# Kernel optimization log

Measured on AMD Instinct MI355X. Metric: run time of the kernel, lower is better.

## Reference

```python
import jax, jax.numpy as jnp
from jax import lax
import numpy as np

DN = ('NCHW', 'OIHW', 'NCHW')

def conv_reflect(x, w, b, pad):
    # torch Conv2d with padding_mode='reflect': reflect-pad then valid conv
    x = jnp.pad(x, ((0, 0), (0, 0), (pad, pad), (pad, pad)), mode='reflect')
    y = lax.conv_general_dilated(x, w, (1, 1), 'VALID', dimension_numbers=DN)
    return y + b[None, :, None, None]

def setup_inputs() -> dict:
    key = jax.random.key(0)
    ks = jax.random.split(key, 8)
    B, W, H = 4, 1024, 1024
    inp = {
        'input': jax.random.normal(ks[0], (B, 12, W, H), dtype=jnp.float32),
        'w1': jax.random.normal(ks[1], (32, 12, 7, 7), dtype=jnp.float32) * 0.05,
        'b1': jnp.zeros((32,), dtype=jnp.float32),
        'w2': jax.random.normal(ks[2], (32, 32, 5, 5), dtype=jnp.float32) * 0.05,
        'b2': jnp.zeros((32,), dtype=jnp.float32),
        'w3': jax.random.normal(ks[3], (8, 32, 5, 5), dtype=jnp.float32) * 0.05,
        'b3': jnp.zeros((8,), dtype=jnp.float32),
        'dwkernel': jax.random.normal(ks[4], (8, 1, 7, 7), dtype=jnp.float32),
    }
    return inp

def reference(input, w1, b1, w2, b2, w3, b3, dwkernel):
    B, _, W, H = input.shape
    color = input[:, 0:3]
    albedo = input[:, 3:6]
    albedo = jnp.where(albedo < 0.001, jnp.float32(1.0), albedo)
    color = color / albedo
    net_in = jnp.concatenate([color, albedo, input[:, 6:]], axis=1)  # (B,12,W,H)

    h = jax.nn.relu(conv_reflect(net_in, w1, b1, 3))
    h = jax.nn.relu(conv_reflect(h, w2, b2, 2))
    logits = conv_reflect(h, w3, b3, 2)  # (B,8,W,H)
    kernel = jax.nn.softmax(logits / 5.0, axis=1)  # (B,8,W,H)

    # grouped conv: dwkernel repeated over 3 color channels, zero padding=3
    rpk = jnp.tile(dwkernel, (3, 1, 1, 1))  # (24,1,7,7)
    preconv = lax.conv_general_dilated(
        color, rpk, (1, 1), [(3, 3), (3, 3)],
        dimension_numbers=DN, feature_group_count=3,
    )  # (B,24,W,H)
    preconv = preconv.reshape(B, 3, 8, W, H)

    # (kernel expanded over color dim * preconv).sum over kernel dim
    filtered = jnp.einsum('bkwh,bckwh->bcwh', kernel, preconv)
    remodulated = albedo * filtered
    return remodulated
```

## Files before the change

kernel.cpp:

```cpp
#include <hip/hip_runtime.h>

#define IMG 1024

typedef _Float16 half8 __attribute__((ext_vector_type(8)));
typedef float f32x4 __attribute__((ext_vector_type(4)));

__device__ __forceinline__ int refl(int i) {
    i = (i < 0) ? -i : i;
    return (i >= IMG) ? (2 * IMG - 2 - i) : i;
}
__device__ __forceinline__ float afix(float a) { return (a < 0.001f) ? 1.0f : a; }
__device__ __forceinline__ int iclamp(int v, int lo, int hi) { return v < lo ? lo : (v > hi ? hi : v); }
__device__ __forceinline__ int swz64(int a) { return a ^ (((((a >> 6) & 3) ^ ((a >> 8) & 1)) << 4)); }
__device__ __forceinline__ int swz32(int a) { return a ^ ((((a >> 7) & 1)) << 4); }
__device__ __forceinline__ unsigned short h2b(_Float16 h) { union { _Float16 f; unsigned short u; } x; x.f = h; return x.u; }

__global__ void wprep_kernel(const float* __restrict__ w1, const float* __restrict__ w2,
                             const float* __restrict__ w3,
                             char* __restrict__ w1p, char* __restrict__ w2p, char* __restrict__ w3p)
{
    const int NF1 = 7 * 2 * 4 * 2, NF2 = 5 * 2 * 5 * 2, NF3 = 5 * 5 * 2;
    int gid = blockIdx.x * 256 + threadIdx.x;
    int f = gid >> 6, l = gid & 63;
    if (f >= NF1 + NF2 + NF3) return;
    int r = l & 15, g = l >> 4;
    half8 out;
    char* dst;
    if (f < NF1) {
        int pl = f & 1, j = (f >> 1) & 3, oct = (f >> 3) & 1, ky = f >> 4;
        int oc = oct * 16 + r;
#pragma unroll
        for (int e = 0; e < 8; e++) {
            int k = g * 8 + e, kx = 2 * j + (k >> 4), ic = k & 15;
            float v = (ic < 12 && kx < 7) ? w1[((oc * 12 + ic) * 7 + ky) * 7 + kx] : 0.f;
            _Float16 h = (_Float16)v;
            out[e] = pl ? (_Float16)(v - (float)h) : h;
        }
        dst = w1p + (size_t)f * 1024 + l * 16;
    } else if (f < NF1 + NF2) {
        int ff = f - NF1;
        int pl = ff & 1, t2 = ff >> 1;
        int kx = t2 % 5; t2 /= 5;
        int oct = t2 & 1, ky = t2 >> 1;
        int oc = oct * 16 + r;
#pragma unroll
        for (int e = 0; e < 8; e++) {
            int ic = g * 8 + e;
            float v = w2[((oc * 32 + ic) * 5 + ky) * 5 + kx];
            _Float16 h = (_Float16)v;
            out[e] = pl ? (_Float16)(v - (float)h) : h;
        }
        dst = w2p + (size_t)ff * 1024 + l * 16;
    } else {
        int ff = f - NF1 - NF2;
        int pl = ff & 1, t2 = ff >> 1;
        int kx = t2 % 5, ky = t2 / 5;
#pragma unroll
        for (int e = 0; e < 8; e++) {
            int ic = g * 8 + e;
            float v = (r < 8) ? w3[((r * 32 + ic) * 5 + ky) * 5 + kx] : 0.f;
            _Float16 h = (_Float16)v;
            out[e] = pl ? (_Float16)(v - (float)h) : h;
        }
        dst = w3p + (size_t)ff * 1024 + l * 16;
    }
    *(half8*)dst = out;
}

__global__ void netin_kernel(const float* __restrict__ in, char* __restrict__ nh, char* __restrict__ nl)
{
    const int M = IMG * IMG;
    int px = blockIdx.x * 256 + threadIdx.x;
    float v[16];
#pragma unroll
    for (int c = 0; c < 3; c++) {
        float a = afix(in[(size_t)(c + 3) * M + px]);
        v[c] = (in[(size_t)c * M + px] / a) * 0.25f;
        v[c + 3] = a * 0.25f;
    }
#pragma unroll
    for (int c = 6; c < 12; c++) v[c] = in[(size_t)c * M + px] * 0.25f;
#pragma unroll
    for (int c = 12; c < 16; c++) v[c] = 0.f;
    unsigned short hb[16], lb[16];
#pragma unroll
    for (int c = 0; c < 16; c++) {
        _Float16 h = (_Float16)v[c];
        hb[c] = h2b(h);
        lb[c] = h2b((_Float16)(v[c] - (float)h));
    }
    *(int4*)(nh + (size_t)px * 32) = *(int4*)&hb[0];
    *(int4*)(nh + (size_t)px * 32 + 16) = *(int4*)&hb[8];
    *(int4*)(nl + (size_t)px * 32) = *(int4*)&lb[0];
    *(int4*)(nl + (size_t)px * 32 + 16) = *(int4*)&lb[8];
}

__global__ __launch_bounds__(256, 2) void conv1_mfma(
    const char* __restrict__ nh, const char* __restrict__ nl,
    const char* __restrict__ w1p, const float* __restrict__ b1,
    char* __restrict__ h1h, char* __restrict__ h1l, int a1, int e1)
{
    __shared__ __align__(16) char sm[2 * 14 * 1280];
    const int t = threadIdx.x, l = t & 63, w = t >> 6;
    const int c = l & 15, g = l >> 4;
    const int x0 = blockIdx.x * 32;
    const int ystart = a1 + blockIdx.y * 8;

    for (int q = t; q < 2240; q += 256) {
        int pl = q / 1120, rem = q % 1120;
        int slab = rem / 80, c2 = rem % 80;
        int px = c2 >> 1, s = c2 & 1;
        int gy = refl(ystart + slab - 3);
        int gx = refl(x0 + px - 3);
        const char* src = (pl ? nl : nh) + ((size_t)gy * IMG + gx) * 32 + s * 16;
        *(int4*)(sm + pl * 17920 + slab * 1280 + swz32(px * 32 + s * 16)) = *(const int4*)src;
    }
    __syncthreads();

    f32x4 zero4 = {0.f, 0.f, 0.f, 0.f};
    f32x4 acc[2][4];
#pragma unroll
    for (int o = 0; o < 2; o++)
#pragma unroll
        for (int r = 0; r < 4; r++) acc[o][r] = zero4;

    const int pxt = w & 1, rbase = (w >> 1) * 4;
#pragma unroll 1
    for (int ky = 0; ky < 7; ky++) {
        half8 aw[2][4][2];
#pragma unroll
        for (int oct = 0; oct < 2; oct++)
#pragma unroll
            for (int j = 0; j < 4; j++)
#pragma unroll
                for (int pl = 0; pl < 2; pl++)
                    aw[oct][j][pl] = *(const half8*)(w1p + (size_t)((((ky * 2 + oct) * 4 + j) * 2 + pl)) * 1024 + l * 16);
#pragma unroll
        for (int r = 0; r < 4; r++) {
            const char* base = sm + (rbase + r + ky) * 1280;
#pragma unroll
            for (int j = 0; j < 4; j++) {
                int p2 = pxt * 16 + c + 2 * j + (g >> 1);
                int off = swz32(p2 * 32 + (g & 1) * 16);
                half8 bh = *(const half8*)(base + off);
                half8 bl = *(const half8*)(base + 17920 + off);
#pragma unroll
                for (int oct = 0; oct < 2; oct++) {
                    acc[oct][r] = __builtin_amdgcn_mfma_f32_16x16x32_f16(aw[oct][j][0], bh, acc[oct][r], 0, 0, 0);
                    acc[oct][r] = __builtin_amdgcn_mfma_f32_16x16x32_f16(aw[oct][j][0], bl, acc[oct][r], 0, 0, 0);
                    acc[oct][r] = __builtin_amdgcn_mfma_f32_16x16x32_f16(aw[oct][j][1], bh, acc[oct][r], 0, 0, 0);
                }
            }
        }
    }
#pragma unroll
    for (int r = 0; r < 4; r++) {
        int y = ystart + rbase + r;
        if (y < e1) {
            int x = x0 + pxt * 16 + c, ybuf = y - a1;
#pragma unroll
            for (int oct = 0; oct < 2; oct++) {
                ushort4 hv, lv;
                float vv[4];
#pragma unroll
                for (int i = 0; i < 4; i++) {
                    int oc = oct * 16 + g * 4 + i;
                    float v = acc[oct][r][i] * 4.f + b1[oc];
                    vv[i] = fmaxf(v, 0.f) * 0.125f;
                }
                _Float16 h0 = (_Float16)vv[0], h1_ = (_Float16)vv[1], h2_ = (_Float16)vv[2], h3 = (_Float16)vv[3];
                hv.x = h2b(h0); hv.y = h2b(h1_); hv.z = h2b(h2_); hv.w = h2b(h3);
                lv.x = h2b((_Float16)(vv[0] - (float)h0)); lv.y = h2b((_Float16)(vv[1] - (float)h1_));
                lv.z = h2b((_Float16)(vv[2] - (float)h2_)); lv.w = h2b((_Float16)(vv[3] - (float)h3));
                size_t ob = ((size_t)ybuf * IMG + x) * 64 + oct * 32 + g * 8;
                *(ushort4*)(h1h + ob) = hv;
                *(ushort4*)(h1l + ob) = lv;
            }
        }
    }
}

__global__ __launch_bounds__(256, 2) void conv2_mfma(
    const char* __restrict__ h1h, const char* __restrict__ h1l,
    const char* __restrict__ w2p, const float* __restrict__ b2,
    char* __restrict__ h2h, char* __restrict__ h2l,
    int a1, int e1, int a2, int e2)
{
    __shared__ __align__(16) char sm[2 * 12 * 2304];
    const int t = threadIdx.x, l = t & 63, w = t >> 6;
    const int c = l & 15, g = l >> 4;
    const int x0 = blockIdx.x * 32;
    const int ystart = a2 + blockIdx.y * 8;

    for (int q = t; q < 3456; q += 256) {
        int pl = q / 1728, rem = q % 1728;
        int slab = rem / 144, c2 = rem % 144;
        int px = c2 >> 2, s = c2 & 3;
        int yy = iclamp(refl(ystart + slab - 2), a1, e1 - 1) - a1;
        int gx = refl(x0 + px - 2);
        const char* src = (pl ? h1l : h1h) + ((size_t)yy * IMG + gx) * 64 + s * 16;
        *(int4*)(sm + pl * 27648 + slab * 2304 + swz64(px * 64 + s * 16)) = *(const int4*)src;
    }
    __syncthreads();

    f32x4 zero4 = {0.f, 0.f, 0.f, 0.f};
    f32x4 acc[2][4];
#pragma unroll
    for (int o = 0; o < 2; o++)
#pragma unroll
        for (int r = 0; r < 4; r++) acc[o][r] = zero4;

    const int pxt = w & 1, rbase = (w >> 1) * 4;
#pragma unroll 1
    for (int ky = 0; ky < 5; ky++) {
        half8 aw[2][5][2];
#pragma unroll
        for (int oct = 0; oct < 2; oct++)
#pragma unroll
            for (int kx = 0; kx < 5; kx++)
#pragma unroll
                for (int pl = 0; pl < 2; pl++)
                    aw[oct][kx][pl] = *(const half8*)(w2p + (size_t)((((ky * 2 + oct) * 5 + kx) * 2 + pl)) * 1024 + l * 16);
#pragma unroll
        for (int r = 0; r < 4; r++) {
            const char* base = sm + (rbase + r + ky) * 2304;
#pragma unroll
            for (int kx = 0; kx < 5; kx++) {
                int p = pxt * 16 + c + kx;
                int off = swz64(p * 64 + g * 16);
                half8 bh = *(const half8*)(base + off);
                half8 bl = *(const half8*)(base + 27648 + off);
#pragma unroll
                for (int oct = 0; oct < 2; oct++) {
                    acc[oct][r] = __builtin_amdgcn_mfma_f32_16x16x32_f16(aw[oct][kx][0], bh, acc[oct][r], 0, 0, 0);
                    acc[oct][r] = __builtin_amdgcn_mfma_f32_16x16x32_f16(aw[oct][kx][0], bl, acc[oct][r], 0, 0, 0);
                    acc[oct][r] = __builtin_amdgcn_mfma_f32_16x16x32_f16(aw[oct][kx][1], bh, acc[oct][r], 0, 0, 0);
                }
            }
        }
    }
#pragma unroll
    for (int r = 0; r < 4; r++) {
        int y = ystart + rbase + r;
        if (y < e2) {
            int x = x0 + pxt * 16 + c, ybuf = y - a2;
#pragma unroll
            for (int oct = 0; oct < 2; oct++) {
                ushort4 hv, lv;
                float vv[4];
#pragma unroll
                for (int i = 0; i < 4; i++) {
                    int oc = oct * 16 + g * 4 + i;
                    float v = acc[oct][r][i] * 8.f + b2[oc];
                    vv[i] = fmaxf(v, 0.f) * 0.125f;
                }
                _Float16 h0 = (_Float16)vv[0], h1_ = (_Float16)vv[1], h2_ = (_Float16)vv[2], h3 = (_Float16)vv[3];
                hv.x = h2b(h0); hv.y = h2b(h1_); hv.z = h2b(h2_); hv.w = h2b(h3);
                lv.x = h2b((_Float16)(vv[0] - (float)h0)); lv.y = h2b((_Float16)(vv[1] - (float)h1_));
                lv.z = h2b((_Float16)(vv[2] - (float)h2_)); lv.w = h2b((_Float16)(vv[3] - (float)h3));
                size_t ob = ((size_t)ybuf * IMG + x) * 64 + oct * 32 + g * 8;
                *(ushort4*)(h2h + ob) = hv;
                *(ushort4*)(h2l + ob) = lv;
            }
        }
    }
}

__global__ __launch_bounds__(256, 2) void conv3_mfma(
    const char* __restrict__ h2h, const char* __restrict__ h2l,
    const char* __restrict__ w3p, const float* __restrict__ b3,
    float* __restrict__ lg, int a2, int e2, int r0, int r1, int rowsL)
{
    __shared__ __align__(16) char sm[2 * 12 * 2304];
    const int t = threadIdx.x, l = t & 63, w = t >> 6;
    const int c = l & 15, g = l >> 4;
    const int x0 = blockIdx.x * 32;
    const int ystart = r0 + blockIdx.y * 8;

    for (int q = t; q < 3456; q += 256) {
        int pl = q / 1728, rem = q % 1728;
        int slab = rem / 144, c2 = rem % 144;
        int px = c2 >> 2, s = c2 & 3;
        int yy = iclamp(refl(ystart + slab - 2), a2, e2 - 1) - a2;
        int gx = refl(x0 + px - 2);
        const char* src = (pl ? h2l : h2h) + ((size_t)yy * IMG + gx) * 64 + s * 16;
        *(int4*)(sm + pl * 27648 + slab * 2304 + swz64(px * 64 + s * 16)) = *(const int4*)src;
    }
    __syncthreads();

    f32x4 zero4 = {0.f, 0.f, 0.f, 0.f};
    f32x4 acc[4];
#pragma unroll
    for (int r = 0; r < 4; r++) acc[r] = zero4;

    const int pxt = w & 1, rbase = (w >> 1) * 4;
#pragma unroll 1
    for (int ky = 0; ky < 5; ky++) {
        half8 aw[5][2];
#pragma unroll
        for (int kx = 0; kx < 5; kx++)
#pragma unroll
            for (int pl = 0; pl < 2; pl++)
                aw[kx][pl] = *(const half8*)(w3p + (size_t)(((ky * 5 + kx) * 2 + pl)) * 1024 + l * 16);
#pragma unroll
        for (int r = 0; r < 4; r++) {
            const char* base = sm + (rbase + r + ky) * 2304;
#pragma unroll
            for (int kx = 0; kx < 5; kx++) {
                int p = pxt * 16 + c + kx;
                int off = swz64(p * 64 + g * 16);
                half8 bh = *(const half8*)(base + off);
                half8 bl = *(const half8*)(base + 27648 + off);
                acc[r] = __builtin_amdgcn_mfma_f32_16x16x32_f16(aw[kx][0], bh, acc[r], 0, 0, 0);
                acc[r] = __builtin_amdgcn_mfma_f32_16x16x32_f16(aw[kx][0], bl, acc[r], 0, 0, 0);
                acc[r] = __builtin_amdgcn_mfma_f32_16x16x32_f16(aw[kx][1], bh, acc[r], 0, 0, 0);
            }
        }
    }
#pragma unroll
    for (int r = 0; r < 4; r++) {
        int y = ystart + rbase + r;
        if (y < r1 && g < 2) {
            int x = x0 + pxt * 16 + c, row = y - r0;
#pragma unroll
            for (int i = 0; i < 4; i++) {
                int oc = g * 4 + i;
                lg[((size_t)oc * rowsL + row) * IMG + x] = acc[r][i] * 8.f + b3[oc];
            }
        }
    }
}

__global__ __launch_bounds__(256, 2) void final_kernel(
    const float* __restrict__ in, const float* __restrict__ lg, const float* __restrict__ dw,
    float* __restrict__ outp, int ylo, int yhi, int rowsL)
{
    __shared__ __align__(16) float sC[3][22][72];
    __shared__ __align__(16) float sdw[8][49];
    const int t = threadIdx.x;
    const int tx = t & 15, ty = t >> 4;
    const int x0 = blockIdx.x * 64;
    const int y0 = ylo + blockIdx.y * 16;

    for (int e = t; e < 8 * 49; e += 256) sdw[e / 49][e % 49] = dw[e];
    for (int e = t; e < 3 * 22 * 70; e += 256) {
        int c = e / (22 * 70), rem = e % (22 * 70);
        int r = rem / 70, cc = rem % 70;
        int gy = y0 + r - 3, gx = x0 + cc - 3;
        float v = 0.f;
        if (gy >= 0 && gy < IMG && gx >= 0 && gx < IMG) {
            float a = afix(in[(size_t)(c + 3) * IMG * IMG + (size_t)gy * IMG + gx]);
            v = in[(size_t)c * IMG * IMG + (size_t)gy * IMG + gx] / a;
        }
        sC[c][r][cc] = v;
    }
    __syncthreads();
    const int y = y0 + ty;
    if (y >= yhi) return;

    float lv[4][8];
#pragma unroll
    for (int k = 0; k < 8; k++) {
        float4 v = *(const float4*)&lg[((size_t)k * rowsL + (y - ylo)) * IMG + x0 + tx * 4];
        lv[0][k] = v.x; lv[1][k] = v.y; lv[2][k] = v.z; lv[3][k] = v.w;
    }
    float p[4][8];
#pragma unroll
    for (int j = 0; j < 4; j++) {
        float m = -3.4e38f;
#pragma unroll
        for (int k = 0; k < 8; k++) m = fmaxf(m, lv[j][k]);
        float s = 0.f;
#pragma unroll
        for (int k = 0; k < 8; k++) { float ev = __expf((lv[j][k] - m) * 0.2f); p[j][k] = ev; s += ev; }
        float invs = 1.0f / s;
#pragma unroll
        for (int k = 0; k < 8; k++) p[j][k] *= invs;
    }

    float filt[3][4];
#pragma unroll
    for (int c = 0; c < 3; c++)
#pragma unroll
        for (int j = 0; j < 4; j++) filt[c][j] = 0.f;

#pragma unroll 1
    for (int ky = 0; ky < 7; ky++) {
        float cv[3][10];
#pragma unroll
        for (int c = 0; c < 3; c++)
#pragma unroll
            for (int jj = 0; jj < 10; jj++) cv[c][jj] = sC[c][ty + ky][tx * 4 + jj];
#pragma unroll
        for (int kx = 0; kx < 7; kx++) {
            float dwv[8];
#pragma unroll
            for (int k = 0; k < 8; k++) dwv[k] = sdw[k][ky * 7 + kx];
#pragma unroll
            for (int j = 0; j < 4; j++) {
                float e0 = 0.f;
#pragma unroll
                for (int k = 0; k < 8; k++) e0 = fmaf(p[j][k], dwv[k], e0);
#pragma unroll
                for (int c = 0; c < 3; c++) filt[c][j] = fmaf(e0, cv[c][kx + j], filt[c][j]);
            }
        }
    }
#pragma unroll
    for (int c = 0; c < 3; c++) {
        const float* ap = &in[(size_t)(c + 3) * IMG * IMG + (size_t)y * IMG + x0 + tx * 4];
        float4 a4 = *(const float4*)ap;
        float4 o4 = make_float4(afix(a4.x) * filt[c][0], afix(a4.y) * filt[c][1],
                                afix(a4.z) * filt[c][2], afix(a4.w) * filt[c][3]);
        *(float4*)&outp[(size_t)c * IMG * IMG + (size_t)y * IMG + x0 + tx * 4] = o4;
    }
}

extern "C" void kernel_launch(void* const* d_in, const int* in_sizes, int n_in,
                              void* d_out, int out_size, void* d_ws, size_t ws_size,
                              hipStream_t stream)
{
    const float* in  = (const float*)d_in[0];
    const float* w1  = (const float*)d_in[1];
    const float* b1  = (const float*)d_in[2];
    const float* w2  = (const float*)d_in[3];
    const float* b2  = (const float*)d_in[4];
    const float* w3  = (const float*)d_in[5];
    const float* b3  = (const float*)d_in[6];
    const float* dw  = (const float*)d_in[7];
    float* out = (float*)d_out;

    const size_t WB1 = 112 * 1024, WB2 = 100 * 1024, WB3 = 50 * 1024;
    const size_t NETIN = (size_t)IMG * IMG * 32;

    int S = 1024;
    while (S > 64) {
        size_t need = WB1 + WB2 + WB3 + 2 * NETIN
                    + 2ull * (S + 8) * IMG * 64 + 2ull * (S + 4) * IMG * 64
                    + (size_t)S * IMG * 8 * 4;
        if (need <= ws_size) break;
        S >>= 1;
    }
    const int rows1 = S + 8, rows2 = S + 4, rowsL = S;

    char* w1p = (char*)d_ws;
    char* w2p = w1p + WB1;
    char* w3p = w2p + WB2;
    char* nh  = w3p + WB3;
    char* nl  = nh + NETIN;
    char* h1h = nl + NETIN;
    char* h1l = h1h + (size_t)rows1 * IMG * 64;
    char* h2h = h1l + (size_t)rows1 * IMG * 64;
    char* h2l = h2h + (size_t)rows2 * IMG * 64;
    float* lgb = (float*)(h2l + (size_t)rows2 * IMG * 64);

    wprep_kernel<<<66, 256, 0, stream>>>(w1, w2, w3, w1p, w2p, w3p);

    for (int b = 0; b < 4; b++) {
        const float* inb = in + (size_t)b * 12 * IMG * IMG;
        float* outb = out + (size_t)b * 3 * IMG * IMG;
        netin_kernel<<<IMG * IMG / 256, 256, 0, stream>>>(inb, nh, nl);
        for (int r0 = 0; r0 < IMG; r0 += S) {
            int r1 = r0 + S; if (r1 > IMG) r1 = IMG;
            int a1 = r0 - 4; if (a1 < 0) a1 = 0;
            int e1 = r1 + 4; if (e1 > IMG) e1 = IMG;
            int a2 = r0 - 2; if (a2 < 0) a2 = 0;
            int e2 = r1 + 2; if (e2 > IMG) e2 = IMG;
            conv1_mfma<<<dim3(32, (e1 - a1 + 7) / 8), 256, 0, stream>>>(nh, nl, w1p, b1, h1h, h1l, a1, e1);
            conv2_mfma<<<dim3(32, (e2 - a2 + 7) / 8), 256, 0, stream>>>(h1h, h1l, w2p, b2, h2h, h2l, a1, e1, a2, e2);
            conv3_mfma<<<dim3(32, (r1 - r0 + 7) / 8), 256, 0, stream>>>(h2h, h2l, w3p, b3, lgb, a2, e2, r0, r1, rowsL);
            final_kernel<<<dim3(16, (r1 - r0 + 15) / 16), 256, 0, stream>>>(inb, lgb, dw, outb, r0, r1, rowsL);
        }
    }
}
```

Baseline: 2.272 ms.

## Split hi/lo activation planes into two sequential LDS passes to halve shared memory

Each conv kernel used to stage both the high and low fp16 planes of its input tile in shared memory at once. Now it stages the high plane, runs the hi×hi and lo-weight×hi MFMAs, then reloads the same buffer with the low plane and runs the hi-weight×lo MFMAs. This halves LDS per block, and launch bounds rise from 2 to 4 blocks per SIMD to buy occupancy. The cost is an extra global-load phase with its own barriers, reloading weights for the second pass, and a tighter register budget that may cause spills.

After: 1.994 ms. 12.2% less time.

```diff
diff --git a/kernel.cpp b/kernel.cpp
--- a/kernel.cpp
+++ b/kernel.cpp
@@ -95,61 +95,87 @@
     *(int4*)(nl + (size_t)px * 32 + 16) = *(int4*)&lb[8];
 }
 
-__global__ __launch_bounds__(256, 2) void conv1_mfma(
+__global__ __launch_bounds__(256, 4) void conv1_mfma(
     const char* __restrict__ nh, const char* __restrict__ nl,
     const char* __restrict__ w1p, const float* __restrict__ b1,
     char* __restrict__ h1h, char* __restrict__ h1l, int a1, int e1)
 {
-    __shared__ __align__(16) char sm[2 * 14 * 1280];
+    __shared__ __align__(16) char sm[14 * 1280];
     const int t = threadIdx.x, l = t & 63, w = t >> 6;
     const int c = l & 15, g = l >> 4;
     const int x0 = blockIdx.x * 32;
     const int ystart = a1 + blockIdx.y * 8;
-
-    for (int q = t; q < 2240; q += 256) {
-        int pl = q / 1120, rem = q % 1120;
-        int slab = rem / 80, c2 = rem % 80;
+    const int pxt = w & 1, rbase = (w >> 1) * 4;
+
+    f32x4 zero4 = {0.f, 0.f, 0.f, 0.f};
+    f32x4 acc[2][4];
+#pragma unroll
+    for (int o = 0; o < 2; o++)
+#pragma unroll
+        for (int r = 0; r < 4; r++) acc[o][r] = zero4;
+
+    for (int q = t; q < 1120; q += 256) {
+        int slab = q / 80, c2 = q % 80;
         int px = c2 >> 1, s = c2 & 1;
         int gy = refl(ystart + slab - 3);
         int gx = refl(x0 + px - 3);
-        const char* src = (pl ? nl : nh) + ((size_t)gy * IMG + gx) * 32 + s * 16;
-        *(int4*)(sm + pl * 17920 + slab * 1280 + swz32(px * 32 + s * 16)) = *(const int4*)src;
-    }
-    __syncthreads();
-
-    f32x4 zero4 = {0.f, 0.f, 0.f, 0.f};
-    f32x4 acc[2][4];
-#pragma unroll
-    for (int o = 0; o < 2; o++)
-#pragma unroll
-        for (int r = 0; r < 4; r++) acc[o][r] = zero4;
-
-    const int pxt = w & 1, rbase = (w >> 1) * 4;
+        *(int4*)(sm + slab * 1280 + swz32(px * 32 + s * 16)) =
+            *(const int4*)(nh + ((size_t)gy * IMG + gx) * 32 + s * 16);
+    }
+    __syncthreads();
 #pragma unroll 1
     for (int ky = 0; ky < 7; ky++) {
-        half8 aw[2][4][2];
+        half8 aw0[2][4], aw1[2][4];
 #pragma unroll
         for (int oct = 0; oct < 2; oct++)
 #pragma unroll
-            for (int j = 0; j < 4; j++)
-#pragma unroll
-                for (int pl = 0; pl < 2; pl++)
-                    aw[oct][j][pl] = *(const half8*)(w1p + (size_t)((((ky * 2 + oct) * 4 + j) * 2 + pl)) * 1024 + l * 16);
+            for (int j = 0; j < 4; j++) {
+                aw0[oct][j] = *(const half8*)(w1p + (size_t)((((ky * 2 + oct) * 4 + j) * 2 + 0)) * 1024 + l * 16);
+                aw1[oct][j] = *(const half8*)(w1p + (size_t)((((ky * 2 + oct) * 4 + j) * 2 + 1)) * 1024 + l * 16);
+            }
 #pragma unroll
         for (int r = 0; r < 4; r++) {
             const char* base = sm + (rbase + r + ky) * 1280;
 #pragma unroll
             for (int j = 0; j < 4; j++) {
                 int p2 = pxt * 16 + c + 2 * j + (g >> 1);
-                int off = swz32(p2 * 32 + (g & 1) * 16);
-                half8 bh = *(const half8*)(base + off);
-                half8 bl = *(const half8*)(base + 17920 + off);
+                half8 bh = *(const half8*)(base + swz32(p2 * 32 + (g & 1) * 16));
 #pragma unroll
                 for (int oct = 0; oct < 2; oct++) {
-                    acc[oct][r] = __builtin_amdgcn_mfma_f32_16x16x32_f16(aw[oct][j][0], bh, acc[oct][r], 0, 0, 0);
-                    acc[oct][r] = __builtin_amdgcn_mfma_f32_16x16x32_f16(aw[oct][j][0], bl, acc[oct][r], 0, 0, 0);
-                    acc[oct][r] = __builtin_amdgcn_mfma_f32_16x16x32_f16(aw[oct][j][1], bh, acc[oct][r], 0, 0, 0);
+                    acc[oct][r] = __builtin_amdgcn_mfma_f32_16x16x32_f16(aw0[oct][j], bh, acc[oct][r], 0, 0, 0);
+                    acc[oct][r] = __builtin_amdgcn_mfma_f32_16x16x32_f16(aw1[oct][j], bh, acc[oct][r], 0, 0, 0);
                 }
+            }
+        }
+    }
+    __syncthreads();
+    for (int q = t; q < 1120; q += 256) {
+        int slab = q / 80, c2 = q % 80;
+        int px = c2 >> 1, s = c2 & 1;
+        int gy = refl(ystart + slab - 3);
+        int gx = refl(x0 + px - 3);
+        *(int4*)(sm + slab * 1280 + swz32(px * 32 + s * 16)) =
+            *(const int4*)(nl + ((size_t)gy * IMG + gx) * 32 + s * 16);
+    }
+    __syncthreads();
+#pragma unroll 1
+    for (int ky = 0; ky < 7; ky++) {
+        half8 aw0[2][4];
+#pragma unroll
+        for (int oct = 0; oct < 2; oct++)
+#pragma unroll
+            for (int j = 0; j < 4; j++)
+                aw0[oct][j] = *(const half8*)(w1p + (size_t)((((ky * 2 + oct) * 4 + j) * 2 + 0)) * 1024 + l * 16);
+#pragma unroll
+        for (int r = 0; r < 4; r++) {
+            const char* base = sm + (rbase + r + ky) * 1280;
+#pragma unroll
+            for (int j = 0; j < 4; j++) {
+                int p2 = pxt * 16 + c + 2 * j + (g >> 1);
+                half8 bl = *(const half8*)(base + swz32(p2 * 32 + (g & 1) * 16));
+#pragma unroll
+                for (int oct = 0; oct < 2; oct++)
+                    acc[oct][r] = __builtin_amdgcn_mfma_f32_16x16x32_f16(aw0[oct][j], bl, acc[oct][r], 0, 0, 0);
             }
         }
     }
@@ -180,62 +206,86 @@
     }
 }
 
-__global__ __launch_bounds__(256, 2) void conv2_mfma(
+__global__ __launch_bounds__(256, 4) void conv2_mfma(
     const char* __restrict__ h1h, const char* __restrict__ h1l,
     const char* __restrict__ w2p, const float* __restrict__ b2,
     char* __restrict__ h2h, char* __restrict__ h2l,
     int a1, int e1, int a2, int e2)
 {
-    __shared__ __align__(16) char sm[2 * 12 * 2304];
+    __shared__ __align__(16) char sm[12 * 2304];
     const int t = threadIdx.x, l = t & 63, w = t >> 6;
     const int c = l & 15, g = l >> 4;
     const int x0 = blockIdx.x * 32;
     const int ystart = a2 + blockIdx.y * 8;
-
-    for (int q = t; q < 3456; q += 256) {
-        int pl = q / 1728, rem = q % 1728;
-        int slab = rem / 144, c2 = rem % 144;
+    const int pxt = w & 1, rbase = (w >> 1) * 4;
+
+    f32x4 zero4 = {0.f, 0.f, 0.f, 0.f};
+    f32x4 acc[2][4];
+#pragma unroll
+    for (int o = 0; o < 2; o++)
+#pragma unroll
+        for (int r = 0; r < 4; r++) acc[o][r] = zero4;
+
+    for (int q = t; q < 1728; q += 256) {
+        int slab = q / 144, c2 = q % 144;
         int px = c2 >> 2, s = c2 & 3;
         int yy = iclamp(refl(ystart + slab - 2), a1, e1 - 1) - a1;
         int gx = refl(x0 + px - 2);
-        const char* src = (pl ? h1l : h1h) + ((size_t)yy * IMG + gx) * 64 + s * 16;
-        *(int4*)(sm + pl * 27648 + slab * 2304 + swz64(px * 64 + s * 16)) = *(const int4*)src;
-    }
-    __syncthreads();
-
-    f32x4 zero4 = {0.f, 0.f, 0.f, 0.f};
-    f32x4 acc[2][4];
-#pragma unroll
-    for (int o = 0; o < 2; o++)
-#pragma unroll
-        for (int r = 0; r < 4; r++) acc[o][r] = zero4;
-
-    const int pxt = w & 1, rbase = (w >> 1) * 4;
+        *(int4*)(sm + slab * 2304 + swz64(px * 64 + s * 16)) =
+            *(const int4*)(h1h + ((size_t)yy * IMG + gx) * 64 + s * 16);
+    }
+    __syncthreads();
 #pragma unroll 1
     for (int ky = 0; ky < 5; ky++) {
-        half8 aw[2][5][2];
+        half8 aw0[2][5], aw1[2][5];
 #pragma unroll
         for (int oct = 0; oct < 2; oct++)
 #pragma unroll
-            for (int kx = 0; kx < 5; kx++)
-#pragma unroll
-                for (int pl = 0; pl < 2; pl++)
-                    aw[oct][kx][pl] = *(const half8*)(w2p + (size_t)((((ky * 2 + oct) * 5 + kx) * 2 + pl)) * 1024 + l * 16);
+            for (int kx = 0; kx < 5; kx++) {
+                aw0[oct][kx] = *(const half8*)(w2p + (size_t)((((ky * 2 + oct) * 5 + kx) * 2 + 0)) * 1024 + l * 16);
+                aw1[oct][kx] = *(const half8*)(w2p + (size_t)((((ky * 2 + oct) * 5 + kx) * 2 + 1)) * 1024 + l * 16);
+            }
 #pragma unroll
         for (int r = 0; r < 4; r++) {
             const char* base = sm + (rbase + r + ky) * 2304;
 #pragma unroll
             for (int kx = 0; kx < 5; kx++) {
-                int p = pxt * 16 + c + kx;
-                int off = swz64(p * 64 + g * 16);
-                half8 bh = *(const half8*)(base + off);
-                half8 bl = *(const half8*)(base + 27648 + off);
+                half8 bh = *(const half8*)(base + swz64((pxt * 16 + c + kx) * 64 + g * 16));
 #pragma unroll
                 for (int oct = 0; oct < 2; oct++) {
-                    acc[oct][r] = __builtin_amdgcn_mfma_f32_16x16x32_f16(aw[oct][kx][0], bh, acc[oct][r], 0, 0, 0);
-                    acc[oct][r] = __builtin_amdgcn_mfma_f32_16x16x32_f16(aw[oct][kx][0], bl, acc[oct][r], 0, 0, 0);
-                    acc[oct][r] = __builtin_amdgcn_mfma_f32_16x16x32_f16(aw[oct][kx][1], bh, acc[oct][r], 0, 0, 0);
+                    acc[oct][r] = __builtin_amdgcn_mfma_f32_16x16x32_f16(aw0[oct][kx], bh, acc[oct][r], 0, 0, 0);
+                    acc[oct][r] = __builtin_amdgcn_mfma_f32_16x16x32_f16(aw1[oct][kx], bh, acc[oct][r], 0, 0, 0);
                 }
+            }
+        }
+    }
+    __syncthreads();
+    for (int q = t; q < 1728; q += 256) {
+        int slab = q / 144, c2 = q % 144;
+        int px = c2 >> 2, s = c2 & 3;
+        int yy = iclamp(refl(ystart + slab - 2), a1, e1 - 1) - a1;
+        int gx = refl(x0 + px - 2);
+        *(int4*)(sm + slab * 2304 + swz64(px * 64 + s * 16)) =
+            *(const int4*)(h1l + ((size_t)yy * IMG + gx) * 64 + s * 16);
+    }
+    __syncthreads();
+#pragma unroll 1
+    for (int ky = 0; ky < 5; ky++) {
+        half8 aw0[2][5];
+#pragma unroll
+        for (int oct = 0; oct < 2; oct++)
+#pragma unroll
+            for (int kx = 0; kx < 5; kx++)
+                aw0[oct][kx] = *(const half8*)(w2p + (size_t)((((ky * 2 + oct) * 5 + kx) * 2 + 0)) * 1024 + l * 16);
+#pragma unroll
+        for (int r = 0; r < 4; r++) {
+            const char* base = sm + (rbase + r + ky) * 2304;
+#pragma unroll
+            for (int kx = 0; kx < 5; kx++) {
+                half8 bl = *(const half8*)(base + swz64((pxt * 16 + c + kx) * 64 + g * 16));
+#pragma unroll
+                for (int oct = 0; oct < 2; oct++)
+                    acc[oct][r] = __builtin_amdgcn_mfma_f32_16x16x32_f16(aw0[oct][kx], bl, acc[oct][r], 0, 0, 0);
             }
         }
     }
@@ -266,54 +316,74 @@
     }
 }
 
-__global__ __launch_bounds__(256, 2) void conv3_mfma(
+__global__ __launch_bounds__(256, 4) void conv3_mfma(
     const char* __restrict__ h2h, const char* __restrict__ h2l,
     const char* __restrict__ w3p, const float* __restrict__ b3,
     float* __restrict__ lg, int a2, int e2, int r0, int r1, int rowsL)
 {
-    __shared__ __align__(16) char sm[2 * 12 * 2304];
+    __shared__ __align__(16) char sm[12 * 2304];
     const int t = threadIdx.x, l = t & 63, w = t >> 6;
     const int c = l & 15, g = l >> 4;
     const int x0 = blockIdx.x * 32;
     const int ystart = r0 + blockIdx.y * 8;
-
-    for (int q = t; q < 3456; q += 256) {
-        int pl = q / 1728, rem = q % 1728;
-        int slab = rem / 144, c2 = rem % 144;
+    const int pxt = w & 1, rbase = (w >> 1) * 4;
+
+    f32x4 zero4 = {0.f, 0.f, 0.f, 0.f};
+    f32x4 acc[4];
+#pragma unroll
+    for (int r = 0; r < 4; r++) acc[r] = zero4;
+
+    for (int q = t; q < 1728; q += 256) {
+        int slab = q / 144, c2 = q % 144;
         int px = c2 >> 2, s = c2 & 3;
         int yy = iclamp(refl(ystart + slab - 2), a2, e2 - 1) - a2;
         int gx = refl(x0 + px - 2);
-        const char* src = (pl ? h2l : h2h) + ((size_t)yy * IMG + gx) * 64 + s * 16;
-        *(int4*)(sm + pl * 27648 + slab * 2304 + swz64(px * 64 + s * 16)) = *(const int4*)src;
-    }
-    __syncthreads();
-
-    f32x4 zero4 = {0.f, 0.f, 0.f, 0.f};
-    f32x4 acc[4];
-#pragma unroll
-    for (int r = 0; r < 4; r++) acc[r] = zero4;
-
-    const int pxt = w & 1, rbase = (w >> 1) * 4;
+        *(int4*)(sm + slab * 2304 + swz64(px * 64 + s * 16)) =
+            *(const int4*)(h2h + ((size_t)yy * IMG + gx) * 64 + s * 16);
+    }
+    __syncthreads();
 #pragma unroll 1
     for (int ky = 0; ky < 5; ky++) {
-        half8 aw[5][2];
-#pragma unroll
-        for (int kx = 0; kx < 5; kx++)
-#pragma unroll
-            for (int pl = 0; pl < 2; pl++)
-                aw[kx][pl] = *(const half8*)(w3p + (size_t)(((ky * 5 + kx) * 2 + pl)) * 1024 + l * 16);
+        half8 aw0[5], aw1[5];
+#pragma unroll
+        for (int kx = 0; kx < 5; kx++) {
+            aw0[kx] = *(const half8*)(w3p + (size_t)(((ky * 5 + kx) * 2 + 0)) * 1024 + l * 16);
+            aw1[kx] = *(const half8*)(w3p + (size_t)(((ky * 5 + kx) * 2 + 1)) * 1024 + l * 16);
+        }
 #pragma unroll
         for (int r = 0; r < 4; r++) {
             const char* base = sm + (rbase + r + ky) * 2304;
 #pragma unroll
             for (int kx = 0; kx < 5; kx++) {
-                int p = pxt * 16 + c + kx;
-                int off = swz64(p * 64 + g * 16);
-                half8 bh = *(const half8*)(base + off);
-                half8 bl = *(const half8*)(base + 27648 + off);
-                acc[r] = __builtin_amdgcn_mfma_f32_16x16x32_f16(aw[kx][0], bh, acc[r], 0, 0, 0);
-                acc[r] = __builtin_amdgcn_mfma_f32_16x16x32_f16(aw[kx][0], bl, acc[r], 0, 0, 0);
-                acc[r] = __builtin_amdgcn_mfma_f32_16x16x32_f16(aw[kx][1], bh, acc[r], 0, 0, 0);
+                half8 bh = *(const half8*)(base + swz64((pxt * 16 + c + kx) * 64 + g * 16));
+                acc[r] = __builtin_amdgcn_mfma_f32_16x16x32_f16(aw0[kx], bh, acc[r], 0, 0, 0);
+                acc[r] = __builtin_amdgcn_mfma_f32_16x16x32_f16(aw1[kx], bh, acc[r], 0, 0, 0);
+            }
+        }
+    }
+    __syncthreads();
+    for (int q = t; q < 1728; q += 256) {
+        int slab = q / 144, c2 = q % 144;
+        int px = c2 >> 2, s = c2 & 3;
+        int yy = iclamp(refl(ystart + slab - 2), a2, e2 - 1) - a2;
+        int gx = refl(x0 + px - 2);
+        *(int4*)(sm + slab * 2304 + swz64(px * 64 + s * 16)) =
+            *(const int4*)(h2l + ((size_t)yy * IMG + gx) * 64 + s * 16);
+    }
+    __syncthreads();
+#pragma unroll 1
+    for (int ky = 0; ky < 5; ky++) {
+        half8 aw0[5];
+#pragma unroll
+        for (int kx = 0; kx < 5; kx++)
+            aw0[kx] = *(const half8*)(w3p + (size_t)(((ky * 5 + kx) * 2 + 0)) * 1024 + l * 16);
+#pragma unroll
+        for (int r = 0; r < 4; r++) {
+            const char* base = sm + (rbase + r + ky) * 2304;
+#pragma unroll
+            for (int kx = 0; kx < 5; kx++) {
+                half8 bl = *(const half8*)(base + swz64((pxt * 16 + c + kx) * 64 + g * 16));
+                acc[r] = __builtin_amdgcn_mfma_f32_16x16x32_f16(aw0[kx], bl, acc[r], 0, 0, 0);
             }
         }
     }
```
